# Performance work log

Hardware: AMD Instinct MI355X
Metric: run time of the kernel (lower is better)

## Reference

```python
import jax, jax.numpy as jnp
import numpy as np

N, E = 50000, 800000
F_IN, EDGE_DIM, H, C = 128, 64, 8, 32
NEG_SLOPE = 0.2


def setup_inputs() -> dict:
    key = jax.random.key(0)
    ks = jax.random.split(key, 9)
    return {
        "x": jax.random.normal(ks[0], (N, F_IN), dtype=jnp.float32),
        "edge_index": jax.random.randint(ks[1], (2, E), 0, N, dtype=jnp.int32),
        "edge_attr": jax.random.normal(ks[2], (E, EDGE_DIM), dtype=jnp.float32),
        "W": jax.random.normal(ks[3], (F_IN, H * C), dtype=jnp.float32) * 0.05,
        "att_src": jax.random.normal(ks[4], (H, C), dtype=jnp.float32) * 0.05,
        "att_dst": jax.random.normal(ks[5], (H, C), dtype=jnp.float32) * 0.05,
        "W_edge": jax.random.normal(ks[6], (EDGE_DIM, H * C), dtype=jnp.float32) * 0.05,
        "att_edge": jax.random.normal(ks[7], (H, C), dtype=jnp.float32) * 0.05,
        "bias": jax.random.normal(ks[8], (H * C,), dtype=jnp.float32) * 0.05,
    }


def reference(x, edge_index, edge_attr, W, att_src, att_dst, W_edge, att_edge, bias):
    src, dst = edge_index[0], edge_index[1]  # messages flow src -> dst
    # Pre-activation ReLU from Graph_intra.forward
    xr = jax.nn.relu(x)
    # Linear projection, per-head view: [N, H, C]
    xs = (xr @ W).reshape(N, H, C)
    # Per-node attention logits: [N, H]
    a_src = jnp.einsum("nhc,hc->nh", xs, att_src)
    a_dst = jnp.einsum("nhc,hc->nh", xs, att_dst)
    # Edge-feature attention contribution: [E, H]
    e_proj = (edge_attr @ W_edge).reshape(E, H, C)
    a_edge = jnp.einsum("ehc,hc->eh", e_proj, att_edge)
    # Per-edge logits + LeakyReLU
    alpha = jax.nn.leaky_relu(a_src[src] + a_dst[dst] + a_edge, NEG_SLOPE)  # [E, H]
    # Segment softmax over destination neighborhoods
    seg_max = jax.ops.segment_max(alpha, dst, num_segments=N)
    seg_max = jnp.where(jnp.isfinite(seg_max), seg_max, 0.0)
    alpha = jnp.exp(alpha - seg_max[dst])
    seg_sum = jax.ops.segment_sum(alpha, dst, num_segments=N)
    alpha = alpha / (seg_sum[dst] + 1e-16)
    # Weighted message aggregation: scatter-add alpha_e * x_src[e]
    msgs = alpha[:, :, None] * xs[src]  # [E, H, C]
    out = jax.ops.segment_sum(msgs, dst, num_segments=N)  # [N, H, C]
    return out.reshape(N, H * C) + bias
```

## Files before the change

kernel.cpp:

```cpp
#include <hip/hip_runtime.h>

#define N_NODES 50000
#define E_EDGES 800000
#define F_IN    128
#define EDGE_DIM 64
#define HC      256
#define NEG_SLOPE 0.2f

typedef __attribute__((ext_vector_type(8))) short short8;
typedef __attribute__((ext_vector_type(4))) float f32x4;

__device__ __forceinline__ unsigned short f2bf(float f) {
    unsigned u = __builtin_bit_cast(unsigned, f);
    u += 0x7fffu + ((u >> 16) & 1u);
    return (unsigned short)(u >> 16);
}
__device__ __forceinline__ float bf2f(unsigned short b) {
    return __builtin_bit_cast(float, (unsigned)b << 16);
}

__global__ __launch_bounds__(256) void k_pre(const float* __restrict__ W,
        const float* __restrict__ att_src, const float* __restrict__ att_dst,
        const float* __restrict__ W_edge, const float* __restrict__ att_edge,
        unsigned short* __restrict__ W_T, unsigned short* __restrict__ WaT,
        float* __restrict__ We_fold, int* __restrict__ counts, int* __restrict__ gcur) {
    int idx = blockIdx.x * 256 + threadIdx.x;
    if (idx < N_NODES) counts[idx] = 0;
    if (idx == 0) *gcur = 0;
    if (idx < 32768) {
        int n = idx >> 7, k = idx & 127;
        W_T[n * 128 + k] = f2bf(W[k * 256 + n]);
    }
    if (idx < 2048) {
        int col = idx & 15, k = idx >> 4;
        const float* att = (col < 8) ? att_src : att_dst;
        int h = col & 7;
        float s = 0.f;
        #pragma unroll
        for (int c = 0; c < 32; ++c)
            s = fmaf(W[k * 256 + h * 32 + c], att[h * 32 + c], s);
        WaT[col * 128 + k] = f2bf(s);
    }
    if (idx < 512) {
        int d = idx >> 3, h = idx & 7;
        float s = 0.f;
        #pragma unroll
        for (int c = 0; c < 32; ++c)
            s = fmaf(W_edge[d * 256 + h * 32 + c], att_edge[h * 32 + c], s);
        We_fold[d * 8 + h] = s;
    }
}

__global__ void k_hist(const int* __restrict__ dst, int* __restrict__ counts) {
    int e = blockIdx.x * 256 + threadIdx.x;
    if (e < E_EDGES) atomicAdd(&counts[dst[e]], 1);
}

#define NT_TILES 782
#define K1_GRID 512
__global__ __launch_bounds__(256, 2) void k1_mfma(const float* __restrict__ x,
        const unsigned short* __restrict__ W_T, const unsigned short* __restrict__ WaT,
        unsigned short* __restrict__ xs, float* __restrict__ a_src, float* __restrict__ a_dst) {
    __shared__ unsigned short sB[256 * 128];
    __shared__ unsigned short sA[64 * 128];
    int t = threadIdx.x;
    for (int G = t; G < 4096; G += 256) {
        int n = G >> 4, gi = G & 15;
        *(int4*)&sB[(n * 16 + (gi ^ (n & 7))) * 8] = *(const int4*)&W_T[n * 128 + gi * 8];
    }
    int lane = t & 63, w = t >> 6, mr = lane & 15, g = lane >> 4;
    short8 wa[4];
    #pragma unroll
    for (int ks = 0; ks < 4; ++ks)
        wa[ks] = *(const short8*)&WaT[mr * 128 + ks * 32 + g * 8];

    bool first = true;
    for (int rt = blockIdx.x; rt < NT_TILES; rt += K1_GRID) {
        if (!first) __syncthreads();
        first = false;
        for (int G = t; G < 1024; G += 256) {
            int r = G >> 4, gi = G & 15;
            int node = rt * 64 + r;
            unsigned short pk[8];
            if (node < N_NODES) {
                const float* xp = &x[(long)node * 128 + gi * 8];
                #pragma unroll
                for (int jj = 0; jj < 8; ++jj) pk[jj] = f2bf(fmaxf(xp[jj], 0.f));
            } else {
                #pragma unroll
                for (int jj = 0; jj < 8; ++jj) pk[jj] = 0;
            }
            *(int4*)&sA[(r * 16 + (gi ^ (r & 7))) * 8] = *(int4*)pk;
        }
        __syncthreads();

        f32x4 acc[17];
        #pragma unroll
        for (int i = 0; i < 17; ++i) acc[i] = (f32x4){0.f, 0.f, 0.f, 0.f};

        int r16 = w * 16 + mr;
        #pragma unroll
        for (int ks = 0; ks < 4; ++ks) {
            int pos = (ks * 4 + g) ^ (mr & 7);
            short8 a = *(const short8*)&sA[(r16 * 16 + pos) * 8];
            #pragma unroll
            for (int nt = 0; nt < 16; ++nt) {
                short8 b = *(const short8*)&sB[((nt * 16 + mr) * 16 + pos) * 8];
                acc[nt] = __builtin_amdgcn_mfma_f32_16x16x32_bf16(a, b, acc[nt], 0, 0, 0);
            }
            acc[16] = __builtin_amdgcn_mfma_f32_16x16x32_bf16(a, wa[ks], acc[16], 0, 0, 0);
        }

        #pragma unroll
        for (int r = 0; r < 4; ++r) {
            int node = rt * 64 + w * 16 + g * 4 + r;
            if (node < N_NODES) {
                #pragma unroll
                for (int nt = 0; nt < 16; ++nt)
                    xs[(long)node * 256 + nt * 16 + mr] = f2bf(acc[nt][r]);
                if (mr < 8) a_src[node * 8 + mr]       = acc[16][r];
                else        a_dst[node * 8 + (mr - 8)] = acc[16][r];
            }
        }
    }
}

__global__ __launch_bounds__(256) void k4_alloc(const int* __restrict__ counts,
                                                int* __restrict__ starts,
                                                int* __restrict__ cursor,
                                                int* __restrict__ gcur) {
    int n = blockIdx.x * 256 + threadIdx.x;
    int c = (n < N_NODES) ? counts[n] : 0;
    int incl = c;
    #pragma unroll
    for (int off = 1; off < 64; off <<= 1) {
        int u = __shfl_up(incl, off);
        if ((threadIdx.x & 63) >= off) incl += u;
    }
    int total = __shfl(incl, 63);
    int wavebase = 0;
    if ((threadIdx.x & 63) == 63) wavebase = atomicAdd(gcur, total);
    wavebase = __shfl(wavebase, 63);
    if (n < N_NODES) {
        int st = wavebase + incl - c;
        starts[n] = st;
        cursor[n] = st;
    }
}

__global__ __launch_bounds__(256) void k25_fused(const float4* __restrict__ edge_attr4,
        const float* __restrict__ We_fold,
        const int* __restrict__ src, const int* __restrict__ dst,
        const float* __restrict__ a_src, const float* __restrict__ a_dst,
        int* __restrict__ cursor,
        float* __restrict__ w_perm, int* __restrict__ src_perm) {
    __shared__ float se[32 * 65];
    __shared__ float sf[512];
    __shared__ int s_src[32], s_dst[32], s_pos[32];
    int t = threadIdx.x;
    long ebase = (long)blockIdx.x * 32;
    for (int i = t; i < 512; i += 256) sf[i] = We_fold[i];
    for (int i = t; i < 512; i += 256) {
        float4 v = edge_attr4[ebase * 16 + i];
        int e = i >> 4, d4 = (i & 15) * 4;
        float* dp = &se[e * 65 + d4];
        dp[0] = v.x; dp[1] = v.y; dp[2] = v.z; dp[3] = v.w;
    }
    if (t < 32) {
        int e = ebase + t;
        int d = dst[e];
        s_src[t] = src[e];
        s_dst[t] = d;
        s_pos[t] = atomicAdd(&cursor[d], 1);
    }
    __syncthreads();
    int e = t >> 3, h = t & 7;
    float s = 0.f;
    #pragma unroll
    for (int d0 = 0; d0 < EDGE_DIM; ++d0)
        s = fmaf(se[e * 65 + d0], sf[d0 * 8 + h], s);
    int sn = s_src[e], dn = s_dst[e];
    float v = a_src[sn * 8 + h] + a_dst[dn * 8 + h] + s;
    v = (v > 0.f) ? v : NEG_SLOPE * v;
    float w = __expf(v);
    int pos = s_pos[e];
    w_perm[(size_t)pos * 8 + h] = w;
    if (h == 0) src_perm[pos] = sn;
}

__global__ __launch_bounds__(256) void k6_wave(
    const int* __restrict__ starts, const int* __restrict__ counts,
    const float* __restrict__ w_perm, const int* __restrict__ src_perm,
    const unsigned short* __restrict__ xs, const float* __restrict__ bias,
    float* __restrict__ out) {
    int lane = threadIdx.x & 63;
    int n = blockIdx.x * 4 + (threadIdx.x >> 6);
    if (n >= N_NODES) return;
    int start = starts[n], cnt = counts[n];
    int j = lane >> 3;
    int hq = lane >> 3;

    float acc0 = 0.f, acc1 = 0.f, acc2 = 0.f, acc3 = 0.f;
    float psum = 0.f;
    for (int base = 0; base < cnt; base += 8) {
        int nk = cnt - base; if (nk > 8) nk = 8;
        float wv = w_perm[(size_t)(start + base) * 8 + lane];
        if (j >= nk) wv = 0.f;
        psum += wv;
        int sv = src_perm[start + base + (lane & 7)];
        #pragma unroll
        for (int jj = 0; jj < 8; ++jj) {
            int s = __shfl(sv, jj);
            s = (jj < nk) ? s : 0;
            float w = __shfl(wv, jj * 8 + hq);
            ushort4 xv = *(const ushort4*)&xs[(size_t)s * 256 + lane * 4];
            acc0 = fmaf(w, bf2f(xv.x), acc0);
            acc1 = fmaf(w, bf2f(xv.y), acc1);
            acc2 = fmaf(w, bf2f(xv.z), acc2);
            acc3 = fmaf(w, bf2f(xv.w), acc3);
        }
    }
    psum += __shfl_xor(psum, 8);
    psum += __shfl_xor(psum, 16);
    psum += __shfl_xor(psum, 32);
    float denom = __shfl(psum, hq);
    float rinv = 1.0f / (denom + 1e-16f);
    float4 bv = *(const float4*)&bias[lane * 4];
    float4 o;
    o.x = acc0 * rinv + bv.x;
    o.y = acc1 * rinv + bv.y;
    o.z = acc2 * rinv + bv.z;
    o.w = acc3 * rinv + bv.w;
    *(float4*)&out[(size_t)n * 256 + lane * 4] = o;
}

extern "C" void kernel_launch(void* const* d_in, const int* in_sizes, int n_in,
                              void* d_out, int out_size, void* d_ws, size_t ws_size,
                              hipStream_t stream) {
    const float* x         = (const float*)d_in[0];
    const int*   ei        = (const int*)d_in[1];
    const float* edge_attr = (const float*)d_in[2];
    const float* W         = (const float*)d_in[3];
    const float* att_src   = (const float*)d_in[4];
    const float* att_dst   = (const float*)d_in[5];
    const float* W_edge    = (const float*)d_in[6];
    const float* att_edge  = (const float*)d_in[7];
    const float* bias      = (const float*)d_in[8];
    float* out = (float*)d_out;

    const int* e_src = ei;
    const int* e_dst = ei + E_EDGES;

    char* p = (char*)d_ws;
    unsigned short* xs = (unsigned short*)p; p += (size_t)N_NODES * HC * 2;
    float* a_src   = (float*)p; p += (size_t)N_NODES * 8 * 4;
    float* a_dst   = (float*)p; p += (size_t)N_NODES * 8 * 4;
    float* w_perm  = (float*)p; p += (size_t)E_EDGES * 8 * 4 + 256;
    int* src_perm  = (int*)p;   p += (size_t)E_EDGES * 4 + 256;
    unsigned short* W_T  = (unsigned short*)p; p += 32768 * 2;
    unsigned short* WaT  = (unsigned short*)p; p += 2048 * 2;
    float* We_fold = (float*)p; p += 512 * 4;
    int* counts    = (int*)p;   p += 200192;
    int* starts    = (int*)p;   p += 200192;
    int* cursor    = (int*)p;   p += 200192;
    int* gcur      = (int*)p;   p += 256;

    hipLaunchKernelGGL(k_pre, dim3(196), dim3(256), 0, stream,
                       W, att_src, att_dst, W_edge, att_edge, W_T, WaT, We_fold, counts, gcur);
    hipLaunchKernelGGL(k_hist, dim3(E_EDGES / 256), dim3(256), 0, stream, e_dst, counts);
    hipLaunchKernelGGL(k1_mfma, dim3(K1_GRID), dim3(256), 0, stream,
                       x, W_T, WaT, xs, a_src, a_dst);
    hipLaunchKernelGGL(k4_alloc, dim3(196), dim3(256), 0, stream,
                       counts, starts, cursor, gcur);
    hipLaunchKernelGGL(k25_fused, dim3(E_EDGES / 32), dim3(256), 0, stream,
                       (const float4*)edge_attr, We_fold, e_src, e_dst,
                       a_src, a_dst, cursor, w_perm, src_perm);
    hipLaunchKernelGGL(k6_wave, dim3(N_NODES / 4), dim3(256), 0, stream,
                       starts, counts, w_perm, src_perm, xs, bias, out);
}
```

Measured before the change: 227.1 us.

## Keep edge-weight fold in registers and reduce edge logits via wave shuffles

The edge-logit kernel no longer stages edge_attr and the folded edge weights through shared memory. Each group of 8 lanes now handles one edge: each lane loads an 8-float slice of the edge features and holds the matching 8x8 slice of the fold matrix in registers. Partial head sums are combined with xor-shuffles, and each lane keeps the result for its own head. Blocks also loop over 8 chunks of 32 edges, so the weight load is amortised and the barrier is gone. The cost is higher register pressure from the 64-float weight array, plus a shuffle reduction per edge.

```diff
diff --git a/kernel.cpp b/kernel.cpp
--- a/kernel.cpp
+++ b/kernel.cpp
@@ -148,44 +148,66 @@
     }
 }
 
+#define K25_ITERS 8
 __global__ __launch_bounds__(256) void k25_fused(const float4* __restrict__ edge_attr4,
-        const float* __restrict__ We_fold,
+        const float4* __restrict__ We_fold4,
         const int* __restrict__ src, const int* __restrict__ dst,
         const float* __restrict__ a_src, const float* __restrict__ a_dst,
         int* __restrict__ cursor,
         float* __restrict__ w_perm, int* __restrict__ src_perm) {
-    __shared__ float se[32 * 65];
-    __shared__ float sf[512];
-    __shared__ int s_src[32], s_dst[32], s_pos[32];
     int t = threadIdx.x;
-    long ebase = (long)blockIdx.x * 32;
-    for (int i = t; i < 512; i += 256) sf[i] = We_fold[i];
-    for (int i = t; i < 512; i += 256) {
-        float4 v = edge_attr4[ebase * 16 + i];
-        int e = i >> 4, d4 = (i & 15) * 4;
-        float* dp = &se[e * 65 + d4];
-        dp[0] = v.x; dp[1] = v.y; dp[2] = v.z; dp[3] = v.w;
-    }
-    if (t < 32) {
-        int e = ebase + t;
-        int d = dst[e];
-        s_src[t] = src[e];
-        s_dst[t] = d;
-        s_pos[t] = atomicAdd(&cursor[d], 1);
-    }
-    __syncthreads();
-    int e = t >> 3, h = t & 7;
-    float s = 0.f;
+    int lane = t & 63;
+    int k = t & 7;
+    int grpLead = lane & 56;
+    float wf[64];
     #pragma unroll
-    for (int d0 = 0; d0 < EDGE_DIM; ++d0)
-        s = fmaf(se[e * 65 + d0], sf[d0 * 8 + h], s);
-    int sn = s_src[e], dn = s_dst[e];
-    float v = a_src[sn * 8 + h] + a_dst[dn * 8 + h] + s;
-    v = (v > 0.f) ? v : NEG_SLOPE * v;
-    float w = __expf(v);
-    int pos = s_pos[e];
-    w_perm[(size_t)pos * 8 + h] = w;
-    if (h == 0) src_perm[pos] = sn;
+    for (int j = 0; j < 16; ++j) {
+        float4 v = We_fold4[k * 16 + j];
+        wf[j * 4 + 0] = v.x; wf[j * 4 + 1] = v.y; wf[j * 4 + 2] = v.z; wf[j * 4 + 3] = v.w;
+    }
+
+    int ebase0 = blockIdx.x * (32 * K25_ITERS);
+    #pragma unroll 1
+    for (int iter = 0; iter < K25_ITERS; ++iter) {
+        int e = ebase0 + iter * 32 + (lane >> 3) + (t >> 6) * 8;
+        int sv = 0, dv = 0, pv = 0;
+        if (k == 0) {
+            sv = src[e];
+            dv = dst[e];
+            pv = atomicAdd(&cursor[dv], 1);
+        }
+        sv = __shfl(sv, grpLead);
+        dv = __shfl(dv, grpLead);
+        pv = __shfl(pv, grpLead);
+        float4 u0 = edge_attr4[(size_t)e * 16 + k * 2];
+        float4 u1 = edge_attr4[(size_t)e * 16 + k * 2 + 1];
+        float p[8];
+        #pragma unroll
+        for (int h = 0; h < 8; ++h) {
+            float s = u0.x * wf[0 * 8 + h];
+            s = fmaf(u0.y, wf[1 * 8 + h], s);
+            s = fmaf(u0.z, wf[2 * 8 + h], s);
+            s = fmaf(u0.w, wf[3 * 8 + h], s);
+            s = fmaf(u1.x, wf[4 * 8 + h], s);
+            s = fmaf(u1.y, wf[5 * 8 + h], s);
+            s = fmaf(u1.z, wf[6 * 8 + h], s);
+            s = fmaf(u1.w, wf[7 * 8 + h], s);
+            p[h] = s;
+        }
+        #pragma unroll
+        for (int r = 1; r < 8; r <<= 1) {
+            #pragma unroll
+            for (int h = 0; h < 8; ++h)
+                p[h] += __shfl_xor(p[h], r);
+        }
+        float ae = (k == 0) ? p[0] : (k == 1) ? p[1] : (k == 2) ? p[2] : (k == 3) ? p[3]
+                 : (k == 4) ? p[4] : (k == 5) ? p[5] : (k == 6) ? p[6] : p[7];
+        float v = ae + a_src[sv * 8 + k] + a_dst[dv * 8 + k];
+        v = (v > 0.f) ? v : NEG_SLOPE * v;
+        float w = __expf(v);
+        w_perm[(size_t)pv * 8 + k] = w;
+        if (k == 0) src_perm[pv] = sv;
+    }
 }
 
 __global__ __launch_bounds__(256) void k6_wave(
@@ -272,8 +294,8 @@
                        x, W_T, WaT, xs, a_src, a_dst);
     hipLaunchKernelGGL(k4_alloc, dim3(196), dim3(256), 0, stream,
                        counts, starts, cursor, gcur);
-    hipLaunchKernelGGL(k25_fused, dim3(E_EDGES / 32), dim3(256), 0, stream,
-                       (const float4*)edge_attr, We_fold, e_src, e_dst,
+    hipLaunchKernelGGL(k25_fused, dim3(E_EDGES / (32 * K25_ITERS)), dim3(256), 0, stream,
+                       (const float4*)edge_attr, (const float4*)We_fold, e_src, e_dst,
                        a_src, a_dst, cursor, w_perm, src_perm);
     hipLaunchKernelGGL(k6_wave, dim3(N_NODES / 4), dim3(256), 0, stream,
                        starts, counts, w_perm, src_perm, xs, bias, out);
```

Result: slower. 238.6 us (+5.1%).

## Split edge slot assignment into separate kernel and gather weights via edge permutation

Applied to the files above, without the earlier changes.

Moves the atomic cursor slot assignment out of the edge-logit kernel into a dedicated k_pos kernel that writes an edge permutation. The edge kernel now writes weights in original edge order (coalesced) instead of scattering them to permuted slots. The aggregation kernel then gathers the edge id, the src index and the weights indirectly through e_perm. This removes scattered writes and the atomic latency from the heavy edge kernel, at the cost of an extra launch and extra indirect, uncoalesced reads in the aggregation stage.

```diff
diff --git a/kernel.cpp b/kernel.cpp
--- a/kernel.cpp
+++ b/kernel.cpp
@@ -148,15 +148,27 @@
     }
 }
 
-__global__ __launch_bounds__(256) void k25_fused(const float4* __restrict__ edge_attr4,
+__global__ __launch_bounds__(256) void k_pos(const int* __restrict__ dst,
+                                             int* __restrict__ cursor,
+                                             int* __restrict__ e_perm) {
+    int e0 = blockIdx.x * 1024 + threadIdx.x;
+    #pragma unroll
+    for (int i = 0; i < 4; ++i) {
+        int e = e0 + i * 256;
+        if (e < E_EDGES) {
+            int p = atomicAdd(&cursor[dst[e]], 1);
+            e_perm[p] = e;
+        }
+    }
+}
+
+__global__ __launch_bounds__(256) void k25_edge(const float4* __restrict__ edge_attr4,
         const float* __restrict__ We_fold,
         const int* __restrict__ src, const int* __restrict__ dst,
         const float* __restrict__ a_src, const float* __restrict__ a_dst,
-        int* __restrict__ cursor,
-        float* __restrict__ w_perm, int* __restrict__ src_perm) {
+        float* __restrict__ w8) {
     __shared__ float se[32 * 65];
     __shared__ float sf[512];
-    __shared__ int s_src[32], s_dst[32], s_pos[32];
     int t = threadIdx.x;
     long ebase = (long)blockIdx.x * 32;
     for (int i = t; i < 512; i += 256) sf[i] = We_fold[i];
@@ -166,31 +178,23 @@
         float* dp = &se[e * 65 + d4];
         dp[0] = v.x; dp[1] = v.y; dp[2] = v.z; dp[3] = v.w;
     }
-    if (t < 32) {
-        int e = ebase + t;
-        int d = dst[e];
-        s_src[t] = src[e];
-        s_dst[t] = d;
-        s_pos[t] = atomicAdd(&cursor[d], 1);
-    }
     __syncthreads();
     int e = t >> 3, h = t & 7;
     float s = 0.f;
     #pragma unroll
     for (int d0 = 0; d0 < EDGE_DIM; ++d0)
         s = fmaf(se[e * 65 + d0], sf[d0 * 8 + h], s);
-    int sn = s_src[e], dn = s_dst[e];
-    float v = a_src[sn * 8 + h] + a_dst[dn * 8 + h] + s;
+    int sn = src[ebase + e];
+    int dn = dst[ebase + e];
+    float v = s + a_src[sn * 8 + h] + a_dst[dn * 8 + h];
     v = (v > 0.f) ? v : NEG_SLOPE * v;
-    float w = __expf(v);
-    int pos = s_pos[e];
-    w_perm[(size_t)pos * 8 + h] = w;
-    if (h == 0) src_perm[pos] = sn;
+    w8[(size_t)(ebase + e) * 8 + h] = __expf(v);
 }
 
 __global__ __launch_bounds__(256) void k6_wave(
     const int* __restrict__ starts, const int* __restrict__ counts,
-    const float* __restrict__ w_perm, const int* __restrict__ src_perm,
+    const int* __restrict__ e_perm, const int* __restrict__ src,
+    const float* __restrict__ w8,
     const unsigned short* __restrict__ xs, const float* __restrict__ bias,
     float* __restrict__ out) {
     int lane = threadIdx.x & 63;
@@ -204,10 +208,14 @@
     float psum = 0.f;
     for (int base = 0; base < cnt; base += 8) {
         int nk = cnt - base; if (nk > 8) nk = 8;
-        float wv = w_perm[(size_t)(start + base) * 8 + lane];
+        int idx = start + base + (lane & 7);
+        if (idx > E_EDGES - 1) idx = E_EDGES - 1;
+        int ev = e_perm[idx];
+        int sv = src[ev];
+        int ej = __shfl(ev, j);
+        float wv = w8[(size_t)ej * 8 + (lane & 7)];
         if (j >= nk) wv = 0.f;
         psum += wv;
-        int sv = src_perm[start + base + (lane & 7)];
         #pragma unroll
         for (int jj = 0; jj < 8; ++jj) {
             int s = __shfl(sv, jj);
@@ -255,8 +263,8 @@
     unsigned short* xs = (unsigned short*)p; p += (size_t)N_NODES * HC * 2;
     float* a_src   = (float*)p; p += (size_t)N_NODES * 8 * 4;
     float* a_dst   = (float*)p; p += (size_t)N_NODES * 8 * 4;
-    float* w_perm  = (float*)p; p += (size_t)E_EDGES * 8 * 4 + 256;
-    int* src_perm  = (int*)p;   p += (size_t)E_EDGES * 4 + 256;
+    float* w8      = (float*)p; p += (size_t)E_EDGES * 8 * 4 + 256;
+    int* e_perm    = (int*)p;   p += (size_t)E_EDGES * 4 + 256;
     unsigned short* W_T  = (unsigned short*)p; p += 32768 * 2;
     unsigned short* WaT  = (unsigned short*)p; p += 2048 * 2;
     float* We_fold = (float*)p; p += 512 * 4;
@@ -272,9 +280,11 @@
                        x, W_T, WaT, xs, a_src, a_dst);
     hipLaunchKernelGGL(k4_alloc, dim3(196), dim3(256), 0, stream,
                        counts, starts, cursor, gcur);
-    hipLaunchKernelGGL(k25_fused, dim3(E_EDGES / 32), dim3(256), 0, stream,
+    hipLaunchKernelGGL(k_pos, dim3((E_EDGES + 1023) / 1024), dim3(256), 0, stream,
+                       e_dst, cursor, e_perm);
+    hipLaunchKernelGGL(k25_edge, dim3(E_EDGES / 32), dim3(256), 0, stream,
                        (const float4*)edge_attr, We_fold, e_src, e_dst,
-                       a_src, a_dst, cursor, w_perm, src_perm);
+                       a_src, a_dst, w8);
     hipLaunchKernelGGL(k6_wave, dim3(N_NODES / 4), dim3(256), 0, stream,
-                       starts, counts, w_perm, src_perm, xs, bias, out);
-}
+                       starts, counts, e_perm, e_src, w8, xs, bias, out);
+}
```

After: 302.1 us. 1.33x slower.
